# Kernel optimization log

Hardware: AMD Instinct MI355X
Metric: run time of the kernel (lower is better)

The kernel has to match this reference:

```python
import jax, jax.numpy as jnp
import numpy as np

B, N, K = 64, 512, 32   # batch, node_num, top_k
D = 64                  # dim == embed_dim == input_dim == out_channels
EPS = 1e-5
NEG_SLOPE = 0.2         # LeakyReLU slope in GraphLayer.message
NEG_INF = -1e9


def setup_inputs() -> dict:
    key = jax.random.key(0)
    ks = jax.random.split(key, 20)
    rn = lambda k, shp, s=1.0: jax.random.normal(k, shp, jnp.float32) * s
    return {
        "data": rn(ks[0], (B, N, D)),
        "org_edge_index": jax.random.randint(ks[1], (2, 1024), 0, N),
        "emb_table": rn(ks[2], (N, D)),                 # nn.Embedding(node_num, dim)
        "lin_W": rn(ks[3], (D, D), 1.0 / np.sqrt(D)),   # GraphLayer.lin (no bias)
        "att_i": rn(ks[4], (D,), 0.1),
        "att_j": rn(ks[5], (D,), 0.1),
        "att_em_i": rn(ks[6], (D,), 0.1),
        "att_em_j": rn(ks[7], (D,), 0.1),
        "gnn_bias": rn(ks[8], (D,), 0.1),
        "bn1_gamma": 1.0 + rn(ks[9], (D,), 0.1),
        "bn1_beta": rn(ks[10], (D,), 0.1),
        "bn1_mean": rn(ks[11], (D,), 0.1),
        "bn1_var": 0.5 + jax.random.uniform(ks[12], (D,), jnp.float32),
        "bno_gamma": 1.0 + rn(ks[13], (D,), 0.1),
        "bno_beta": rn(ks[14], (D,), 0.1),
        "bno_mean": rn(ks[15], (D,), 0.1),
        "bno_var": 0.5 + jax.random.uniform(ks[16], (D,), jnp.float32),
        "out_W": rn(ks[17], (1, D), 1.0 / np.sqrt(D)),  # OutLayer single Linear(dim,1)
        "out_b": rn(ks[18], (1,), 0.1),
    }


def _gdn_forward(data, emb_table, lin_W, att_i, att_j, att_em_i, att_em_j, gnn_bias,
                 bn1_gamma, bn1_beta, bn1_mean, bn1_var,
                 bno_gamma, bno_beta, bno_mean, bno_var, out_W, out_b):
    Bn, Nn, Fin = data.shape
    x = data.reshape(-1, Fin)                               # [B*N, Fin]

    # --- dynamic graph: cosine-sim topk on detached embedding ---
    w = jax.lax.stop_gradient(emb_table)                    # weights_arr = emb.detach()
    nrm = jnp.linalg.norm(w, axis=-1)
    cos = (w @ w.T) / (nrm[:, None] * nrm[None, :])         # [N, N]
    topk_idx = jax.lax.top_k(cos, K)[1]                     # [N, K]
    src0 = topk_idx.reshape(-1)                             # j (sources)
    dst0 = jnp.repeat(jnp.arange(Nn), K)                    # i (targets)
    valid0 = src0 != dst0                                   # remove_self_loops
    offs = (jnp.arange(Bn) * Nn)[:, None]
    src = (src0[None, :] + offs).reshape(-1)                # [B*N*K]
    dst = (dst0[None, :] + offs).reshape(-1)
    valid = jnp.tile(valid0, Bn)
    loops = jnp.arange(Bn * Nn)                             # add_self_loops
    src = jnp.concatenate([src, loops])
    dst = jnp.concatenate([dst, loops])
    valid = jnp.concatenate([valid, jnp.ones(Bn * Nn, bool)])

    # --- GraphLayer (heads=1, concat=False) ---
    xl = x @ lin_W.T                                        # [B*N, D]
    src_l = src % Nn                                        # embedding tiled over batch
    dst_l = dst % Nn
    a = (xl[dst] @ att_i + emb_table[dst_l] @ att_em_i
         + xl[src] @ att_j + emb_table[src_l] @ att_em_j)   # [E]
    a = jnp.where(a >= 0, a, NEG_SLOPE * a)                 # leaky_relu
    a = jnp.where(valid, a, NEG_INF)
    seg = Bn * Nn
    amax = jax.ops.segment_max(a, dst, num_segments=seg)    # stable softmax per target
    ex = jnp.where(valid, jnp.exp(a - amax[dst]), 0.0)
    denom = jax.ops.segment_sum(ex, dst, num_segments=seg)
    alpha = ex / denom[dst]                                 # [E]
    agg = jax.ops.segment_sum(xl[src] * alpha[:, None], dst, num_segments=seg) + gnn_bias

    # --- GNNLayer BN (eval) + relu ---
    h = (agg - bn1_mean) / jnp.sqrt(bn1_var + EPS) * bn1_gamma + bn1_beta
    h = jax.nn.relu(h).reshape(Bn, Nn, -1)

    # --- mul by node embedding, BN over channels (eval), relu, dropout(eval)=id ---
    h = h * emb_table[None]
    h = (h - bno_mean) / jnp.sqrt(bno_var + EPS) * bno_gamma + bno_beta
    h = jax.nn.relu(h)

    # --- OutLayer: single Linear(dim, 1) ---
    out = h @ out_W.T + out_b                               # [B, N, 1]
    return out.reshape(-1, Nn)                              # [B, N]


def reference(data, org_edge_index, emb_table, lin_W, att_i, att_j, att_em_i, att_em_j,
              gnn_bias, bn1_gamma, bn1_beta, bn1_mean, bn1_var,
              bno_gamma, bno_beta, bno_mean, bno_var, out_W, out_b):
    # org_edge_index is accepted but unused by GDN.forward (dynamic graph replaces it)
    del org_edge_index
    return _gdn_forward(data, emb_table, lin_W, att_i, att_j, att_em_i, att_em_j, gnn_bias,
                        bn1_gamma, bn1_beta, bn1_mean, bn1_var,
                        bno_gamma, bno_beta, bno_mean, bno_var, out_W, out_b)
```

## Files before the change

kernel.cpp:

```cpp
#include <hip/hip_runtime.h>
#include <hip/hip_bf16.h>
#include <math.h>

#define BB 64
#define NN 512
#define KK 32
#define DD 64
#define BN (BB*NN)
#define EPSC 1e-5f
#define NEG_SLOPE 0.2f
#define NEG_INF_A (-1e9f)

typedef unsigned long long ull;


__global__ void kA_cos(const float* __restrict__ emb, ull* __restrict__ keys) {
    __shared__ float4 As[256];
    __shared__ float4 Bs[1024];
    __shared__ float rsA[16];
    const int t = threadIdx.x;
    const int lane = t & 63;
    const int wave = t >> 6;
    const int bi = blockIdx.x >> 3;
    const int c0 = (blockIdx.x & 7) * 64;
    const float4* emb4 = (const float4*)emb;

    As[t] = emb4[bi*256 + t];
    #pragma unroll
    for (int p = 0; p < 4; ++p) {
        const int idx = t + 256*p;
        const int r = idx >> 4, q = idx & 15;
        Bs[(r<<4) | (q ^ (r & 15))] = emb4[c0*16 + idx];
    }
    __syncthreads();

    if (wave == 0) {
        const int r = lane >> 2, qq = lane & 3;
        float ss = 0.f;
        #pragma unroll
        for (int m = 0; m < 4; ++m) {
            const float4 a = As[r*16 + qq*4 + m];
            ss += a.x*a.x + a.y*a.y + a.z*a.z + a.w*a.w;
        }
        ss += __shfl_xor(ss, 1);
        ss += __shfl_xor(ss, 2);
        if (qq == 0) rsA[r] = rsqrtf(ss);
    }

    float4 Wr[16];
    float ssW = 0.f;
    #pragma unroll
    for (int q = 0; q < 16; ++q) {
        Wr[q] = Bs[(lane<<4) | (q ^ (lane & 15))];
        ssW += Wr[q].x*Wr[q].x + Wr[q].y*Wr[q].y + Wr[q].z*Wr[q].z + Wr[q].w*Wr[q].w;
    }
    const float rsW = rsqrtf(ssW);
    __syncthreads();

    #pragma unroll
    for (int r = 0; r < 4; ++r) {
        const int jr = wave*4 + r;
        float acc = 0.f;
        #pragma unroll
        for (int q = 0; q < 16; ++q) {
            const float4 a = As[jr*16 + q];
            const float4 w = Wr[q];
            acc += a.x*w.x + a.y*w.y + a.z*w.z + a.w*w.w;
        }
        const float c = acc * rsA[jr] * rsW;
        const int row = bi*16 + jr;
        const int col = c0 + lane;
        unsigned int u = __float_as_uint(c);
        u = (u & 0x80000000u) ? ~u : (u | 0x80000000u);
        keys[row*NN + col] = ((ull)u << 16) | (ull)(NN - 1 - col);
    }
}

__global__ void kB_rank(const ull* __restrict__ keys,
                        const float* __restrict__ emb,
                        const float* __restrict__ att_em_i,
                        const float* __restrict__ att_em_j,
                        const float* __restrict__ gnn_bias,
                        const float* __restrict__ g1, const float* __restrict__ b1,
                        const float* __restrict__ m1, const float* __restrict__ v1,
                        const float* __restrict__ go, const float* __restrict__ bo,
                        const float* __restrict__ mo, const float* __restrict__ vo,
                        int* __restrict__ topk,
                        float* __restrict__ ei, float* __restrict__ ej,
                        float* __restrict__ epi) {
    __shared__ ull ks[NN];
    const int i = blockIdx.x;
    const int t = threadIdx.x;
    ks[t] = keys[i*NN + t];

    if (t < DD) {
        const float e = emb[i*DD + t];
        float e1 = e * att_em_i[t];
        float e2 = e * att_em_j[t];
        #pragma unroll
        for (int m = 32; m > 0; m >>= 1) {
            e1 += __shfl_xor(e1, m);
            e2 += __shfl_xor(e2, m);
        }
        if (t == 0) { ei[i] = e1; ej[i] = e2; }
    }
    if (i == 0 && t >= 64 && t < 64 + DD) {
        const int d = t - 64;
        float s1 = g1[d] / sqrtf(v1[d] + EPSC);
        float B1 = (gnn_bias[d] - m1[d]) * s1 + b1[d];
        float so = go[d] / sqrtf(vo[d] + EPSC);
        float Bo = bo[d] - mo[d] * so;
        epi[d] = s1; epi[DD + d] = B1; epi[2*DD + d] = so; epi[3*DD + d] = Bo;
    }
    __syncthreads();
    const ull mykey = ks[t];
    int rank = 0;
    #pragma unroll 16
    for (int kk = 0; kk < NN; ++kk) rank += (ks[kk] > mykey) ? 1 : 0;
    if (rank < KK) topk[i*KK + rank] = t;
}

__global__ void k2_lin(const float* __restrict__ data,
                       const float* __restrict__ linW,
                       const float* __restrict__ att_i, const float* __restrict__ att_j,
                       const float* __restrict__ ei, const float* __restrict__ ej,
                       float* __restrict__ xl, float* __restrict__ si,
                       float* __restrict__ sj) {
    __shared__ float4 Ws[1024];
    __shared__ float4 xs[512];
    const int t = threadIdx.x;
    const int lane = t & 63;
    const int wave = t >> 6;
    const float4* W4 = (const float4*)linW;

    const int bid = blockIdx.x;
    const int xcd = bid & 7;
    const int j   = bid >> 3;
    const int batch = xcd + 8 * (j >> 4);
    const int sub   = j & 15;
    const int row0  = batch * NN + sub * 32;

    #pragma unroll
    for (int p = 0; p < 4; ++p) {
        const int idx = t + 256*p;
        const int r = idx >> 4, q = idx & 15;
        Ws[(r<<4) | (q ^ (r & 15))] = W4[idx];
    }
    xs[t]       = ((const float4*)data)[row0*16 + t];
    xs[t + 256] = ((const float4*)data)[row0*16 + t + 256];
    __syncthreads();

    float4 Wr[16];
    #pragma unroll
    for (int q = 0; q < 16; ++q) Wr[q] = Ws[(lane<<4) | (q ^ (lane & 15))];

    const int r0 = wave * 8;
    float acc[8] = {0.f, 0.f, 0.f, 0.f, 0.f, 0.f, 0.f, 0.f};
    #pragma unroll
    for (int q = 0; q < 16; ++q) {
        const float4 w = Wr[q];
        #pragma unroll
        for (int r = 0; r < 8; ++r) {
            const float4 x = xs[(r0+r)*16 + q];
            acc[r] += x.x*w.x + x.y*w.y + x.z*w.z + x.w*w.w;
        }
    }

    const int vbase = row0 + r0;
    #pragma unroll
    for (int r = 0; r < 8; ++r) xl[(vbase+r)*DD + lane] = acc[r];

    const float ai = att_i[lane];
    const float aj = att_j[lane];
    #pragma unroll
    for (int r = 0; r < 8; ++r) {
        float pi = acc[r] * ai;
        float pj = acc[r] * aj;
        #pragma unroll
        for (int m = 32; m > 0; m >>= 1) {
            pi += __shfl_xor(pi, m);
            pj += __shfl_xor(pj, m);
        }
        if (lane == 0) {
            const int v = vbase + r;
            si[v] = pi + ei[v & (NN-1)];
            sj[v] = pj + ej[v & (NN-1)];
        }
    }
}

__global__ void k3_agg(const float* __restrict__ xl, const float* __restrict__ si,
                       const float* __restrict__ sj, const int* __restrict__ topk,
                       const float* __restrict__ emb,
                       const float* __restrict__ epi,
                       const float* __restrict__ outW, const float* __restrict__ outb,
                       float* __restrict__ out) {
    const int t = threadIdx.x;
    const int lane = t & 63;
    const int wave = t >> 6;
    const int bid = blockIdx.x;
    const int xcd = bid & 7;
    const int ixc = bid >> 3;
    const int b   = xcd + 8 * (ixc >> 7);
    const int i   = ((ixc & 127) << 2) + wave;
    const int tgt = b * NN + i;

    const bool isedge = (lane <= KK);
    int tk = i;
    bool valid = true;
    if (lane < KK) { tk = topk[i*KK + lane]; valid = (tk != i); }
    const int srcg = b * NN + tk;

    float a;
    if (isedge) {
        a = si[tgt] + sj[srcg];
        a = (a >= 0.f) ? a : NEG_SLOPE * a;
        if (!valid) a = NEG_INF_A;
    } else {
        a = -3.0e38f;
    }

    float amax = a;
    #pragma unroll
    for (int m = 32; m > 0; m >>= 1) amax = fmaxf(amax, __shfl_xor(amax, m));

    float ex = (isedge && valid) ? __expf(a - amax) : 0.f;
    float denom = ex;
    #pragma unroll
    for (int m = 32; m > 0; m >>= 1) denom += __shfl_xor(denom, m);
    const float alpha = ex * __builtin_amdgcn_rcpf(denom);

    const int c4 = lane & 15;
    const int e4 = lane >> 4;
    const float4* xl4 = (const float4*)xl;

    float al[9];
    int   off[9];
    #pragma unroll
    for (int m = 0; m < 8; ++m) {
        const int kk = 4*m + e4;
        al[m]  = __shfl(alpha, kk);
        off[m] = __shfl(srcg, kk)*16 + c4;
    }
    const float alpha32 = __shfl(alpha, KK);
    const int   srcg32  = __shfl(srcg, KK);
    al[8]  = (e4 == 0) ? alpha32 : 0.f;
    off[8] = srcg32*16 + c4;

    float4 xv[9];
    #pragma unroll
    for (int m = 0; m < 9; ++m) xv[m] = xl4[off[m]];

    float4 acc = make_float4(0.f, 0.f, 0.f, 0.f);
    #pragma unroll
    for (int m = 0; m < 9; ++m) {
        acc.x += al[m]*xv[m].x; acc.y += al[m]*xv[m].y;
        acc.z += al[m]*xv[m].z; acc.w += al[m]*xv[m].w;
    }

    #pragma unroll
    for (int m = 16; m <= 32; m <<= 1) {
        acc.x += __shfl_xor(acc.x, m);
        acc.y += __shfl_xor(acc.y, m);
        acc.z += __shfl_xor(acc.z, m);
        acc.w += __shfl_xor(acc.w, m);
    }

    const float4* epi4 = (const float4*)epi;
    const float4 s1 = epi4[c4];
    const float4 B1 = epi4[16 + c4];
    const float4 so = epi4[32 + c4];
    const float4 Bo = epi4[48 + c4];
    const float4 em = ((const float4*)emb)[i*16 + c4];
    const float4 w4 = ((const float4*)outW)[c4];
    float4 h;
    h.x = fmaxf(acc.x*s1.x + B1.x, 0.f) * em.x;
    h.y = fmaxf(acc.y*s1.y + B1.y, 0.f) * em.y;
    h.z = fmaxf(acc.z*s1.z + B1.z, 0.f) * em.z;
    h.w = fmaxf(acc.w*s1.w + B1.w, 0.f) * em.w;
    h.x = fmaxf(h.x*so.x + Bo.x, 0.f);
    h.y = fmaxf(h.y*so.y + Bo.y, 0.f);
    h.z = fmaxf(h.z*so.z + Bo.z, 0.f);
    h.w = fmaxf(h.w*so.w + Bo.w, 0.f);
    float p = h.x*w4.x + h.y*w4.y + h.z*w4.z + h.w*w4.w;
    p += __shfl_xor(p, 1);
    p += __shfl_xor(p, 2);
    p += __shfl_xor(p, 4);
    p += __shfl_xor(p, 8);
    if (lane == 0) out[tgt] = p + outb[0];
}

extern "C" void kernel_launch(void* const* d_in, const int* in_sizes, int n_in,
                              void* d_out, int out_size, void* d_ws, size_t ws_size,
                              hipStream_t stream) {
    (void)in_sizes; (void)n_in; (void)out_size; (void)ws_size;
    const float* data   = (const float*)d_in[0];
    const float* emb    = (const float*)d_in[2];
    const float* linW   = (const float*)d_in[3];
    const float* att_i  = (const float*)d_in[4];
    const float* att_j  = (const float*)d_in[5];
    const float* attemi = (const float*)d_in[6];
    const float* attemj = (const float*)d_in[7];
    const float* gbias  = (const float*)d_in[8];
    const float* g1     = (const float*)d_in[9];
    const float* b1     = (const float*)d_in[10];
    const float* m1     = (const float*)d_in[11];
    const float* v1     = (const float*)d_in[12];
    const float* go     = (const float*)d_in[13];
    const float* bo     = (const float*)d_in[14];
    const float* mo     = (const float*)d_in[15];
    const float* vo     = (const float*)d_in[16];
    const float* outW   = (const float*)d_in[17];
    const float* outb   = (const float*)d_in[18];
    float* out = (float*)d_out;

    char* ws = (char*)d_ws;
    float* ei   = (float*)(ws + 0);
    float* ej   = (float*)(ws + 4096);
    float* epi  = (float*)(ws + 8192);
    int*   topk = (int*)  (ws + 16384);
    float* si   = (float*)(ws + 81920);
    float* sj   = (float*)(ws + 212992);
    float* xl   = (float*)(ws + 344064);
    ull*   keys = (ull*)  (ws + 344064);

    kA_cos<<<256, 256, 0, stream>>>(emb, keys);
    kB_rank<<<NN, NN, 0, stream>>>(keys, emb, attemi, attemj, gbias,
                                   g1, b1, m1, v1, go, bo, mo, vo,
                                   topk, ei, ej, epi);
    k2_lin<<<BN/32, 256, 0, stream>>>(data, linW, att_i, att_j, ei, ej,
                                      xl, si, sj);
    k3_agg<<<BN/4, 256, 0, stream>>>(xl, si, sj, topk, emb, epi,
                                     outW, outb, out);
}
```

Measured before the change: 136.2 us.

## Merge cosine-topk and linear projection into one heterogeneous prep kernel

Combines the three front kernels (cosine similarity, rank-based top-k, linear projection) into a single launch. Blocks 0-1023 run the linear projection and now fold the embedding attention terms directly into si/sj, while blocks 1024-1535 each compute one row of cosine similarities into shared memory and rank them to pick top-k. This removes two kernel launches, the global keys buffer round-trip, and the ei/ej intermediates. The cost is that each top-k block recomputes all 512 row norms from global memory, and mixing two block roles in one grid can unbalance scheduling.

```diff
diff --git a/kernel.cpp b/kernel.cpp
--- a/kernel.cpp
+++ b/kernel.cpp
@@ -1,5 +1,4 @@
 #include <hip/hip_runtime.h>
-#include <hip/hip_bf16.h>
 #include <math.h>
 
 #define BB 64
@@ -14,177 +13,143 @@
 typedef unsigned long long ull;
 
 
-__global__ void kA_cos(const float* __restrict__ emb, ull* __restrict__ keys) {
-    __shared__ float4 As[256];
-    __shared__ float4 Bs[1024];
-    __shared__ float rsA[16];
-    const int t = threadIdx.x;
-    const int lane = t & 63;
-    const int wave = t >> 6;
-    const int bi = blockIdx.x >> 3;
-    const int c0 = (blockIdx.x & 7) * 64;
-    const float4* emb4 = (const float4*)emb;
-
-    As[t] = emb4[bi*256 + t];
-    #pragma unroll
-    for (int p = 0; p < 4; ++p) {
-        const int idx = t + 256*p;
-        const int r = idx >> 4, q = idx & 15;
-        Bs[(r<<4) | (q ^ (r & 15))] = emb4[c0*16 + idx];
-    }
-    __syncthreads();
-
-    if (wave == 0) {
-        const int r = lane >> 2, qq = lane & 3;
-        float ss = 0.f;
-        #pragma unroll
-        for (int m = 0; m < 4; ++m) {
-            const float4 a = As[r*16 + qq*4 + m];
-            ss += a.x*a.x + a.y*a.y + a.z*a.z + a.w*a.w;
-        }
-        ss += __shfl_xor(ss, 1);
-        ss += __shfl_xor(ss, 2);
-        if (qq == 0) rsA[r] = rsqrtf(ss);
-    }
-
-    float4 Wr[16];
-    float ssW = 0.f;
-    #pragma unroll
-    for (int q = 0; q < 16; ++q) {
-        Wr[q] = Bs[(lane<<4) | (q ^ (lane & 15))];
-        ssW += Wr[q].x*Wr[q].x + Wr[q].y*Wr[q].y + Wr[q].z*Wr[q].z + Wr[q].w*Wr[q].w;
-    }
-    const float rsW = rsqrtf(ssW);
-    __syncthreads();
-
-    #pragma unroll
-    for (int r = 0; r < 4; ++r) {
-        const int jr = wave*4 + r;
-        float acc = 0.f;
-        #pragma unroll
-        for (int q = 0; q < 16; ++q) {
-            const float4 a = As[jr*16 + q];
-            const float4 w = Wr[q];
-            acc += a.x*w.x + a.y*w.y + a.z*w.z + a.w*w.w;
-        }
-        const float c = acc * rsA[jr] * rsW;
-        const int row = bi*16 + jr;
-        const int col = c0 + lane;
-        unsigned int u = __float_as_uint(c);
-        u = (u & 0x80000000u) ? ~u : (u | 0x80000000u);
-        keys[row*NN + col] = ((ull)u << 16) | (ull)(NN - 1 - col);
-    }
-}
-
-__global__ void kB_rank(const ull* __restrict__ keys,
+__global__ void k1_prep(const float* __restrict__ data,
+                        const float* __restrict__ linW,
                         const float* __restrict__ emb,
-                        const float* __restrict__ att_em_i,
-                        const float* __restrict__ att_em_j,
+                        const float* __restrict__ att_i,
+                        const float* __restrict__ att_j,
+                        const float* __restrict__ attemi,
+                        const float* __restrict__ attemj,
                         const float* __restrict__ gnn_bias,
                         const float* __restrict__ g1, const float* __restrict__ b1,
                         const float* __restrict__ m1, const float* __restrict__ v1,
                         const float* __restrict__ go, const float* __restrict__ bo,
                         const float* __restrict__ mo, const float* __restrict__ vo,
-                        int* __restrict__ topk,
-                        float* __restrict__ ei, float* __restrict__ ej,
+                        float* __restrict__ xl, float* __restrict__ si,
+                        float* __restrict__ sj, int* __restrict__ topk,
                         float* __restrict__ epi) {
-    __shared__ ull ks[NN];
-    const int i = blockIdx.x;
+    __shared__ __align__(16) char smem[24576];
     const int t = threadIdx.x;
-    ks[t] = keys[i*NN + t];
-
-    if (t < DD) {
-        const float e = emb[i*DD + t];
-        float e1 = e * att_em_i[t];
-        float e2 = e * att_em_j[t];
-        #pragma unroll
-        for (int m = 32; m > 0; m >>= 1) {
-            e1 += __shfl_xor(e1, m);
-            e2 += __shfl_xor(e2, m);
-        }
-        if (t == 0) { ei[i] = e1; ej[i] = e2; }
-    }
-    if (i == 0 && t >= 64 && t < 64 + DD) {
-        const int d = t - 64;
-        float s1 = g1[d] / sqrtf(v1[d] + EPSC);
-        float B1 = (gnn_bias[d] - m1[d]) * s1 + b1[d];
-        float so = go[d] / sqrtf(vo[d] + EPSC);
-        float Bo = bo[d] - mo[d] * so;
-        epi[d] = s1; epi[DD + d] = B1; epi[2*DD + d] = so; epi[3*DD + d] = Bo;
-    }
-    __syncthreads();
-    const ull mykey = ks[t];
-    int rank = 0;
-    #pragma unroll 16
-    for (int kk = 0; kk < NN; ++kk) rank += (ks[kk] > mykey) ? 1 : 0;
-    if (rank < KK) topk[i*KK + rank] = t;
-}
-
-__global__ void k2_lin(const float* __restrict__ data,
-                       const float* __restrict__ linW,
-                       const float* __restrict__ att_i, const float* __restrict__ att_j,
-                       const float* __restrict__ ei, const float* __restrict__ ej,
-                       float* __restrict__ xl, float* __restrict__ si,
-                       float* __restrict__ sj) {
-    __shared__ float4 Ws[1024];
-    __shared__ float4 xs[512];
-    const int t = threadIdx.x;
-    const int lane = t & 63;
-    const int wave = t >> 6;
-    const float4* W4 = (const float4*)linW;
-
     const int bid = blockIdx.x;
-    const int xcd = bid & 7;
-    const int j   = bid >> 3;
-    const int batch = xcd + 8 * (j >> 4);
-    const int sub   = j & 15;
-    const int row0  = batch * NN + sub * 32;
-
-    #pragma unroll
-    for (int p = 0; p < 4; ++p) {
-        const int idx = t + 256*p;
-        const int r = idx >> 4, q = idx & 15;
-        Ws[(r<<4) | (q ^ (r & 15))] = W4[idx];
-    }
-    xs[t]       = ((const float4*)data)[row0*16 + t];
-    xs[t + 256] = ((const float4*)data)[row0*16 + t + 256];
-    __syncthreads();
-
-    float4 Wr[16];
-    #pragma unroll
-    for (int q = 0; q < 16; ++q) Wr[q] = Ws[(lane<<4) | (q ^ (lane & 15))];
-
-    const int r0 = wave * 8;
-    float acc[8] = {0.f, 0.f, 0.f, 0.f, 0.f, 0.f, 0.f, 0.f};
-    #pragma unroll
-    for (int q = 0; q < 16; ++q) {
-        const float4 w = Wr[q];
+
+    if (bid < 1024) {
+        float4* Ws = (float4*)smem;
+        float4* xs = (float4*)(smem + 16384);
+        const int lane = t & 63;
+        const int wave = t >> 6;
+        const float4* W4 = (const float4*)linW;
+
+        const int xcd = bid & 7;
+        const int j   = bid >> 3;
+        const int batch = xcd + 8 * (j >> 4);
+        const int sub   = j & 15;
+        const int row0  = batch * NN + sub * 32;
+
+        #pragma unroll
+        for (int p = 0; p < 4; ++p) {
+            const int idx = t + 256*p;
+            const int r = idx >> 4, q = idx & 15;
+            Ws[(r<<4) | (q ^ (r & 15))] = W4[idx];
+        }
+        xs[t]       = ((const float4*)data)[row0*16 + t];
+        xs[t + 256] = ((const float4*)data)[row0*16 + t + 256];
+        __syncthreads();
+
+        float4 Wr[16];
+        #pragma unroll
+        for (int q = 0; q < 16; ++q) Wr[q] = Ws[(lane<<4) | (q ^ (lane & 15))];
+
+        const int r0 = wave * 8;
+        float acc[8] = {0.f, 0.f, 0.f, 0.f, 0.f, 0.f, 0.f, 0.f};
+        #pragma unroll
+        for (int q = 0; q < 16; ++q) {
+            const float4 w = Wr[q];
+            #pragma unroll
+            for (int r = 0; r < 8; ++r) {
+                const float4 x = xs[(r0+r)*16 + q];
+                acc[r] += x.x*w.x + x.y*w.y + x.z*w.z + x.w*w.w;
+            }
+        }
+
+        const int vbase = row0 + r0;
+        #pragma unroll
+        for (int r = 0; r < 8; ++r) xl[(vbase+r)*DD + lane] = acc[r];
+
+        const float ai  = att_i[lane];
+        const float aj  = att_j[lane];
+        const float aei = attemi[lane];
+        const float aej = attemj[lane];
+        const int node0 = sub*32 + r0;
         #pragma unroll
         for (int r = 0; r < 8; ++r) {
-            const float4 x = xs[(r0+r)*16 + q];
-            acc[r] += x.x*w.x + x.y*w.y + x.z*w.z + x.w*w.w;
-        }
-    }
-
-    const int vbase = row0 + r0;
-    #pragma unroll
-    for (int r = 0; r < 8; ++r) xl[(vbase+r)*DD + lane] = acc[r];
-
-    const float ai = att_i[lane];
-    const float aj = att_j[lane];
-    #pragma unroll
-    for (int r = 0; r < 8; ++r) {
-        float pi = acc[r] * ai;
-        float pj = acc[r] * aj;
-        #pragma unroll
-        for (int m = 32; m > 0; m >>= 1) {
-            pi += __shfl_xor(pi, m);
-            pj += __shfl_xor(pj, m);
-        }
-        if (lane == 0) {
-            const int v = vbase + r;
-            si[v] = pi + ei[v & (NN-1)];
-            sj[v] = pj + ej[v & (NN-1)];
+            const float em = emb[(node0 + r)*DD + lane];
+            float pi = acc[r]*ai + em*aei;
+            float pj = acc[r]*aj + em*aej;
+            #pragma unroll
+            for (int m = 32; m > 0; m >>= 1) {
+                pi += __shfl_xor(pi, m);
+                pj += __shfl_xor(pj, m);
+            }
+            if (lane == 0) {
+                const int v = vbase + r;
+                si[v] = pi;
+                sj[v] = pj;
+            }
+        }
+    } else {
+        const int i = bid - 1024;
+        ull*    ks = (ull*)smem;
+        float4* Ai = (float4*)(smem + 4096);
+
+        if (t < 16) Ai[t] = ((const float4*)emb)[i*16 + t];
+        __syncthreads();
+
+        float4 Af[16];
+        float ssA = 0.f;
+        #pragma unroll
+        for (int q = 0; q < 16; ++q) {
+            Af[q] = Ai[q];
+            ssA += Af[q].x*Af[q].x + Af[q].y*Af[q].y + Af[q].z*Af[q].z + Af[q].w*Af[q].w;
+        }
+        const float rsA = rsqrtf(ssA);
+        const float4* e4 = (const float4*)emb;
+
+        #pragma unroll
+        for (int half = 0; half < 2; ++half) {
+            const int jc = t + 256*half;
+            float acc = 0.f, ss = 0.f;
+            #pragma unroll
+            for (int q = 0; q < 16; ++q) {
+                const float4 w = e4[jc*16 + q];
+                acc += Af[q].x*w.x + Af[q].y*w.y + Af[q].z*w.z + Af[q].w*w.w;
+                ss  += w.x*w.x + w.y*w.y + w.z*w.z + w.w*w.w;
+            }
+            const float c = acc * rsA * rsqrtf(ss);
+            unsigned int u = __float_as_uint(c);
+            u = (u & 0x80000000u) ? ~u : (u | 0x80000000u);
+            ks[jc] = ((ull)u << 16) | (ull)(NN - 1 - jc);
+        }
+        __syncthreads();
+
+        const ull k1 = ks[t];
+        const ull k2 = ks[t + 256];
+        int r1 = 0, r2 = 0;
+        #pragma unroll 16
+        for (int kk = 0; kk < NN; ++kk) {
+            const ull kv = ks[kk];
+            r1 += (kv > k1) ? 1 : 0;
+            r2 += (kv > k2) ? 1 : 0;
+        }
+        if (r1 < KK) topk[i*KK + r1] = t;
+        if (r2 < KK) topk[i*KK + r2] = t + 256;
+
+        if (i == 0 && t < DD) {
+            const int d = t;
+            const float s1 = g1[d] / sqrtf(v1[d] + EPSC);
+            const float B1 = (gnn_bias[d] - m1[d]) * s1 + b1[d];
+            const float so = go[d] / sqrtf(vo[d] + EPSC);
+            const float Bo = bo[d] - mo[d] * so;
+            epi[d] = s1; epi[DD + d] = B1; epi[2*DD + d] = so; epi[3*DD + d] = Bo;
         }
     }
 }
@@ -315,21 +280,16 @@
     float* out = (float*)d_out;
 
     char* ws = (char*)d_ws;
-    float* ei   = (float*)(ws + 0);
-    float* ej   = (float*)(ws + 4096);
     float* epi  = (float*)(ws + 8192);
     int*   topk = (int*)  (ws + 16384);
     float* si   = (float*)(ws + 81920);
     float* sj   = (float*)(ws + 212992);
     float* xl   = (float*)(ws + 344064);
-    ull*   keys = (ull*)  (ws + 344064);
-
-    kA_cos<<<256, 256, 0, stream>>>(emb, keys);
-    kB_rank<<<NN, NN, 0, stream>>>(keys, emb, attemi, attemj, gbias,
-                                   g1, b1, m1, v1, go, bo, mo, vo,
-                                   topk, ei, ej, epi);
-    k2_lin<<<BN/32, 256, 0, stream>>>(data, linW, att_i, att_j, ei, ej,
-                                      xl, si, sj);
+
+    k1_prep<<<1536, 256, 0, stream>>>(data, linW, emb, att_i, att_j,
+                                      attemi, attemj, gbias,
+                                      g1, b1, m1, v1, go, bo, mo, vo,
+                                      xl, si, sj, topk, epi);
     k3_agg<<<BN/4, 256, 0, stream>>>(xl, si, sj, topk, emb, epi,
                                      outW, outb, out);
 }
```

After: 136.2 us. No clear change (-0.0%).
